# Kernel optimization log

Measured on AMD Instinct MI355X. Metric: run time of the kernel, lower is better.

Reference implementation:

```python
import jax, jax.numpy as jnp
import numpy as np
import math

C = 256
N_HEAD = 8
GROUPS = 16
EPS = 1e-5


def group_norm(x, w, b):
    # x: [B, C, H, W]; biased variance over (group_channels, H, W), like torch GroupNorm
    B, Cc, H, W = x.shape
    xg = x.reshape(B, GROUPS, Cc // GROUPS, H, W)
    mean = xg.mean(axis=(2, 3, 4), keepdims=True)
    var = ((xg - mean) ** 2).mean(axis=(2, 3, 4), keepdims=True)
    xn = ((xg - mean) * jax.lax.rsqrt(var + EPS)).reshape(B, Cc, H, W)
    return xn * w[None, :, None, None] + b[None, :, None, None]


def setup_inputs() -> dict:
    key = jax.random.key(0)
    k0, k1, k2, k3, k4, k5 = jax.random.split(key, 6)
    B, H, W = 4, 48, 48
    input_feat = jax.random.normal(k0, (B, C, H, W), dtype=jnp.float32)
    gn_weight = jnp.ones((C,), dtype=jnp.float32) + 0.02 * jax.random.normal(k1, (C,), dtype=jnp.float32)
    gn_bias = 0.02 * jax.random.normal(k2, (C,), dtype=jnp.float32)
    w_qkv = jax.random.normal(k3, (3 * C, C), dtype=jnp.float32) / math.sqrt(C)  # Conv2d 1x1, no bias
    w_out = jax.random.normal(k4, (C, C), dtype=jnp.float32) / math.sqrt(C)      # Conv2d 1x1
    b_out = 0.02 * jax.random.normal(k5, (C,), dtype=jnp.float32)
    return {"input_feat": input_feat, "gn_weight": gn_weight, "gn_bias": gn_bias,
            "w_qkv": w_qkv, "w_out": w_out, "b_out": b_out}


def reference(input_feat, gn_weight, gn_bias, w_qkv, w_out, b_out):
    # H=W=48 <= max_attn_size=48 -> full attention branch
    B, Cc, H, W = input_feat.shape
    n, d = N_HEAD, Cc // N_HEAD
    S = H * W
    normed = group_norm(input_feat, gn_weight, gn_bias)
    # 1x1 conv QKV: [B, 3C, H, W]
    qkv = jnp.einsum('oc,bchw->bohw', w_qkv, normed)
    # view(B, n, 3*d, H, W).chunk(3, dim=2) == reshape to (B, n, 3, d, S)
    qkv = qkv.reshape(B, n, 3, d, S)
    q, k, v = qkv[:, :, 0], qkv[:, :, 1], qkv[:, :, 2]  # each [B, n, d, S]
    # NOTE: original divides by sqrt(channel), not sqrt(head_dim)
    scale = 1.0 / math.sqrt(Cc)
    scores = jnp.einsum('bnds,bndt->bnst', q, k) * scale  # [B, n, S, S]
    attn = jax.nn.softmax(scores, axis=-1)
    o = jnp.einsum('bnst,bndt->bnds', attn, v)  # [B, n, d, S]
    o = o.reshape(B, Cc, H, W)
    out = jnp.einsum('oc,bchw->bohw', w_out, o) + b_out[None, :, None, None]
    return out + input_feat
```

## Files before the change

kernel.cpp:

```cpp
#include <hip/hip_runtime.h>
#include <hip/hip_bf16.h>
#include <stdint.h>

#define S    2304
#define CHN  256
#define BATCH 4
#define NKEYS 1152
#define QS   0.09016844005556021f

typedef __attribute__((ext_vector_type(8))) short bf16x8;
typedef __attribute__((ext_vector_type(4))) float f32x4;
typedef __attribute__((ext_vector_type(2))) uint32_t u32x2;
typedef __attribute__((ext_vector_type(4))) unsigned short u16x4;
typedef unsigned short u16;

#define AS1 __attribute__((address_space(1)))
#define AS3 __attribute__((address_space(3)))
#define GLDS(gptr, lptr) __builtin_amdgcn_global_load_lds((const AS1 void*)(gptr), (AS3 void*)(lptr), 16, 0, 0)

__device__ __forceinline__ u16 f2bf(float f) {
  union { float f; uint32_t u; } v; v.f = f;
  uint32_t u = v.u;
  u += 0x7fffu + ((u >> 16) & 1u);
  return (u16)(u >> 16);
}
__device__ __forceinline__ float bf2f(u16 h) {
  union { uint32_t u; float f; } v; v.u = ((uint32_t)h) << 16;
  return v.f;
}
__device__ __forceinline__ uint32_t pk_bf16(float a, float b) {
  union { __hip_bfloat162 h; uint32_t u; } cv;
  cv.h = __float22bfloat162_rn(make_float2(a, b));
  return cv.u;
}

__global__ void k_prep(const float* __restrict__ wq, const float* __restrict__ wo,
                       u16* __restrict__ wq_bf, u16* __restrict__ wo_bf,
                       float* __restrict__ sraw) {
  int i = blockIdx.x * 256 + threadIdx.x;
  if (blockIdx.x == 0 && threadIdx.x < 128) sraw[threadIdx.x] = 0.f;
  if (i < 768 * 256) wq_bf[i] = f2bf(wq[i]);
  int j = i - 768 * 256;
  if (j >= 0 && j < 256 * 256) wo_bf[j] = f2bf(wo[j]);
}

__global__ void k_gnstats(const float* __restrict__ x, float* __restrict__ sraw) {
  int blk = blockIdx.x;
  int bg = blk >> 2, part = blk & 3;
  const float4* p = (const float4*)(x + (size_t)bg * 36864) + part * 2304;
  float s = 0.f, ss = 0.f;
  for (int i = threadIdx.x; i < 2304; i += 256) {
    float4 v = p[i];
    s  += v.x + v.y + v.z + v.w;
    ss += v.x * v.x + v.y * v.y + v.z * v.z + v.w * v.w;
  }
  int lane = threadIdx.x & 63, wv = threadIdx.x >> 6;
  for (int m = 1; m < 64; m <<= 1) { s += __shfl_xor(s, m, 64); ss += __shfl_xor(ss, m, 64); }
  __shared__ float rs[4], rss[4];
  if (lane == 0) { rs[wv] = s; rss[wv] = ss; }
  __syncthreads();
  if (threadIdx.x == 0) {
    float S_ = rs[0] + rs[1] + rs[2] + rs[3];
    float SS = rss[0] + rss[1] + rss[2] + rss[3];
    atomicAdd(&sraw[bg * 2], S_);
    atomicAdd(&sraw[bg * 2 + 1], SS);
  }
}

__global__ void k_gnnorm(const float* __restrict__ x, const float* __restrict__ w,
                         const float* __restrict__ bias, const float* __restrict__ sraw,
                         u16* __restrict__ nt) {
  int bid = blockIdx.x;
  int b = bid / 144, r = bid % 144;
  int sblk = r >> 2, cq = r & 3;
  int t = threadIdx.x;
  int ni = t & 63, cgrp = t >> 6;
  int s = sblk * 64 + ni;
  int cbase = cq * 64 + cgrp * 16;
  int bgi = b * 16 + (cbase >> 4);
  float sx = sraw[bgi * 2], ssx = sraw[bgi * 2 + 1];
  float mean = sx * (1.f / 36864.f);
  float var  = ssx * (1.f / 36864.f) - mean * mean;
  float rstd = rsqrtf(var + 1e-5f);
  bf16x8 v0, v1;
  #pragma unroll
  for (int e = 0; e < 16; ++e) {
    int c = cbase + e;
    float val = x[(size_t)(b * 256 + c) * S + s];
    float xn = (val - mean) * rstd * w[c] + bias[c];
    if (e < 8) v0[e] = (short)f2bf(xn); else v1[e - 8] = (short)f2bf(xn);
  }
  u16* dst = nt + (size_t)(b * S + s) * 256 + cbase;
  *(bf16x8*)dst = v0;
  *(bf16x8*)(dst + 8) = v1;
}

__global__ __launch_bounds__(256) void k_qkv(const u16* __restrict__ A,
                                             const u16* __restrict__ Bm,
                                             u16* __restrict__ qkt,
                                             u16* __restrict__ vt) {
  __shared__ __align__(16) u16 As[2][64 * 32];
  __shared__ __align__(16) u16 Bs[2][128 * 32];
  int tid = threadIdx.x, lane = tid & 63, w = tid >> 6;
  int wr = w >> 1, wc = w & 1;
  int cb = lane & 15, q4 = lane >> 4;
  int m0 = blockIdx.y * 64, n0 = blockIdx.x * 128;

  const u16* gA0 = A  + (size_t)(m0 + (tid >> 2)) * 256 + (tid & 3) * 8;
  const u16* gB0 = Bm + (size_t)(n0 + (tid >> 2)) * 256 + (tid & 3) * 8;
  const u16* gB1 = gB0 + 64 * 256;
  char* lA = (char*)&As[0][0] + (w << 10);
  char* lB = (char*)&Bs[0][0] + (w << 10);

  #define STAGE_Q(buf, k0) do {                      \
    GLDS(gA0 + (k0), lA + (buf) * 4096);             \
    GLDS(gB0 + (k0), lB + (buf) * 8192);             \
    GLDS(gB1 + (k0), lB + (buf) * 8192 + 4096);      \
  } while (0)

  f32x4 zero4 = {0.f, 0.f, 0.f, 0.f};
  f32x4 acc[2][4];
  for (int i = 0; i < 2; ++i) for (int j = 0; j < 4; ++j) acc[i][j] = zero4;

  STAGE_Q(0, 0);
  __syncthreads();
  for (int ks = 0; ks < 8; ++ks) {
    int cur = ks & 1;
    if (ks < 7) STAGE_Q(cur ^ 1, (ks + 1) * 32);
    const u16* as = &As[cur][0];
    const u16* bs = &Bs[cur][0];
    bf16x8 af[2], bfr[4];
    for (int i = 0; i < 2; ++i)
      af[i]  = *(const bf16x8*)&as[(wr * 32 + i * 16 + cb) * 32 + 8 * q4];
    for (int j = 0; j < 4; ++j)
      bfr[j] = *(const bf16x8*)&bs[(wc * 64 + j * 16 + cb) * 32 + 8 * q4];
    for (int i = 0; i < 2; ++i)
      for (int j = 0; j < 4; ++j)
        acc[i][j] = __builtin_amdgcn_mfma_f32_16x16x32_bf16(af[i], bfr[j], acc[i][j], 0, 0, 0);
    __syncthreads();
  }

  for (int i = 0; i < 2; ++i)
    for (int j = 0; j < 4; ++j) {
      int ob = m0 + wr * 32 + i * 16 + q4 * 4;
      int n  = n0 + wc * 64 + j * 16 + cb;
      int h = ob / 96, oq = ob % 96;
      if (oq < 64) {
        float sc = (oq < 32) ? QS : 1.f;
        u16x4 pk;
        for (int r = 0; r < 4; ++r) pk[r] = f2bf(acc[i][j][r] * sc);
        *(u16x4*)&qkt[(size_t)n * 512 + h * 64 + oq] = pk;
      } else {
        for (int r = 0; r < 4; ++r)
          vt[(size_t)(h * 32 + oq - 64 + r) * 9216 + n] = f2bf(acc[i][j][r]);
      }
    }
  #undef STAGE_Q
}

__global__ __launch_bounds__(512) void k_attn(const u16* __restrict__ qkt,
                                              const u16* __restrict__ vt,
                                              u16* __restrict__ ot) {
  __shared__ __align__(16) u16 Ks[2][2][2048];
  __shared__ __align__(16) u16 Vd[2][2][2048];
  __shared__ __align__(16) u16 Ps[8][1024];
  __shared__ float Ls[8][16];

  int tid = threadIdx.x, lane = tid & 63, w = tid >> 6;
  int cb = lane & 15, g4 = lane >> 4;
  int qw = w & 3, half = w >> 2;
  int hw = blockIdx.x;
  int orig = (hw & 7) * 144 + (hw >> 3);
  int bh = orig / 36, qtile = orig % 36;
  int b = bh >> 3, h = bh & 7;
  int q0 = qtile * 64 + qw * 16;

  const u16* kbase = qkt + (size_t)(b * S) * 512 + h * 64 + 32 + (size_t)half * NKEYS * 512;
  const u16* vbase = vt + (size_t)(h * 32) * 9216 + (size_t)b * S + half * NKEYS;

  bf16x8 qf = *(const bf16x8*)&qkt[(size_t)(b * S + q0 + cb) * 512 + h * 64 + 8 * g4];
  bf16x8 vones;
  #pragma unroll
  for (int e = 0; e < 8; ++e) vones[e] = (short)0x3F80;

  f32x4 zero4 = {0.f, 0.f, 0.f, 0.f};
  f32x4 acc_o[2]; acc_o[0] = zero4; acc_o[1] = zero4;
  f32x4 lacc4 = zero4;

  int xk = (cb ^ (cb >> 2)) & 3;
  int sw7 = cb & 7;

  const u16* p_kf[4];
  #pragma unroll
  for (int k4 = 0; k4 < 4; ++k4)
    p_kf[k4] = &Ks[half][0][(16 * k4 + cb) * 32 + ((g4 ^ xk) * 8)];
  u16* p_pw[4];
  #pragma unroll
  for (int k4 = 0; k4 < 4; ++k4)
    p_pw[k4] = &Ps[w][cb * 64 + (((2 * k4 + (g4 >> 1)) ^ sw7) << 3) + ((g4 & 1) << 2)];
  const u16* p_pa[2];
  #pragma unroll
  for (int kk = 0; kk < 2; ++kk)
    p_pa[kk] = &Ps[w][cb * 64 + (((4 * kk + g4) ^ sw7) << 3)];
  const u16* p_vb[2][2];
  #pragma unroll
  for (int jd = 0; jd < 2; ++jd)
    #pragma unroll
    for (int kk = 0; kk < 2; ++kk)
      p_vb[jd][kk] = &Vd[half][0][(16 * jd + cb) * 64 + (((4 * kk + g4) ^ sw7) << 3)];

  int tloc = tid & 255;
  int krow = tloc >> 2, kch = (tloc & 3) ^ ((krow ^ (krow >> 2)) & 3);
  int vrow = tloc >> 3, vch = (tloc & 7) ^ (vrow & 7);
  const u16* gK = kbase + (size_t)krow * 512 + kch * 8;
  const u16* gV = vbase + (size_t)vrow * 9216 + vch * 8;
  char* ldsK = (char*)&Ks[half][0][0] + (qw << 10);
  char* ldsV = (char*)&Vd[half][0][0] + (qw << 10);

  #define STAGE_A(buf) do {                          \
    GLDS(gK, ldsK + (buf) * 4096);                   \
    GLDS(gV, ldsV + (buf) * 4096);                   \
    gK += 64 * 512; gV += 64;                        \
  } while (0)

  #define TILE(buf, pf) do {                                                   \
    if (pf) STAGE_A(buf ^ 1);                                                  \
    bf16x8 kf[4];                                                              \
    _Pragma("unroll")                                                          \
    for (int k4 = 0; k4 < 4; ++k4)                                             \
      kf[k4] = *(const bf16x8*)(p_kf[k4] + (buf) * 2048);                      \
    f32x4 pacc[4];                                                             \
    __builtin_amdgcn_s_setprio(1);                                             \
    _Pragma("unroll")                                                          \
    for (int k4 = 0; k4 < 4; ++k4)                                             \
      pacc[k4] = __builtin_amdgcn_mfma_f32_16x16x32_bf16(kf[k4], qf, zero4, 0, 0, 0); \
    __builtin_amdgcn_s_setprio(0);                                             \
    _Pragma("unroll")                                                          \
    for (int k4 = 0; k4 < 4; ++k4) {                                           \
      f32x4 p = pacc[k4];                                                      \
      float e0 = __builtin_amdgcn_exp2f(p[0]);                                 \
      float e1 = __builtin_amdgcn_exp2f(p[1]);                                 \
      float e2 = __builtin_amdgcn_exp2f(p[2]);                                 \
      float e3 = __builtin_amdgcn_exp2f(p[3]);                                 \
      u32x2 pk = { pk_bf16(e0, e1), pk_bf16(e2, e3) };                         \
      *(u32x2*)p_pw[k4] = pk;                                                  \
    }                                                                          \
    asm volatile("s_waitcnt lgkmcnt(0)" ::: "memory");                         \
    __builtin_amdgcn_sched_barrier(0);                                         \
    __builtin_amdgcn_s_setprio(1);                                             \
    bf16x8 pa[2];                                                              \
    _Pragma("unroll")                                                          \
    for (int kk = 0; kk < 2; ++kk)                                             \
      pa[kk] = *(const bf16x8*)p_pa[kk];                                       \
    lacc4 = __builtin_amdgcn_mfma_f32_16x16x32_bf16(pa[0], vones, lacc4, 0, 0, 0); \
    lacc4 = __builtin_amdgcn_mfma_f32_16x16x32_bf16(pa[1], vones, lacc4, 0, 0, 0); \
    _Pragma("unroll")                                                          \
    for (int jd = 0; jd < 2; ++jd)                                             \
      _Pragma("unroll")                                                        \
      for (int kk = 0; kk < 2; ++kk) {                                         \
        bf16x8 vb = *(const bf16x8*)(p_vb[jd][kk] + (buf) * 2048);             \
        acc_o[jd] = __builtin_amdgcn_mfma_f32_16x16x32_bf16(pa[kk], vb, acc_o[jd], 0, 0, 0); \
      }                                                                        \
    __builtin_amdgcn_s_setprio(0);                                             \
    __syncthreads();                                                           \
  } while (0)

  STAGE_A(0);
  __syncthreads();
  for (int it = 0; it < 9; ++it) {
    TILE(0, 1);
    TILE(1, it < 8);
  }

  float* PsF = (float*)&Ps[w][0];
  #pragma unroll
  for (int jd = 0; jd < 2; ++jd)
    *(f32x4*)&PsF[(cb + 16 * jd) * 16 + 4 * g4] = acc_o[jd];
  if (cb == 0)
    *(f32x4*)&Ls[w][4 * g4] = lacc4;
  __syncthreads();

  const float* A0 = (const float*)&Ps[qw][0];
  const float* A1 = (const float*)&Ps[qw + 4][0];
  int dd = half * 16 + cb;
  f32x4 s0 = *(const f32x4*)&A0[dd * 16 + 4 * g4];
  f32x4 s1 = *(const f32x4*)&A1[dd * 16 + 4 * g4];
  f32x4 lt0 = *(const f32x4*)&Ls[qw][4 * g4];
  f32x4 lt1 = *(const f32x4*)&Ls[qw + 4][4 * g4];
  #pragma unroll
  for (int r = 0; r < 4; ++r) {
    float inv = __builtin_amdgcn_rcpf(lt0[r] + lt1[r]);
    int sq = q0 + 4 * g4 + r;
    ot[(size_t)(b * S + sq) * 256 + h * 32 + dd] = f2bf((s0[r] + s1[r]) * inv);
  }
  #undef STAGE_A
  #undef TILE
}

__global__ __launch_bounds__(256) void k_oproj(const u16* __restrict__ A,
                                               const u16* __restrict__ Bm,
                                               float* __restrict__ out,
                                               const float* __restrict__ bias,
                                               const float* __restrict__ resid) {
  __shared__ __align__(16) u16 As[2][64 * 32];
  __shared__ __align__(16) u16 Bs[2][64 * 32];
  int tid = threadIdx.x, lane = tid & 63, w = tid >> 6;
  int cb = lane & 15, q4 = lane >> 4;
  int m0 = blockIdx.y * 64, n0 = blockIdx.x * 64;

  const u16* gA0 = A  + (size_t)(m0 + (tid >> 2)) * 256 + (tid & 3) * 8;
  const u16* gB0 = Bm + (size_t)(n0 + (tid >> 2)) * 256 + (tid & 3) * 8;
  char* lA = (char*)&As[0][0] + (w << 10);
  char* lB = (char*)&Bs[0][0] + (w << 10);

  #define STAGE_O(buf, k0) do {                      \
    GLDS(gA0 + (k0), lA + (buf) * 4096);             \
    GLDS(gB0 + (k0), lB + (buf) * 4096);             \
  } while (0)

  f32x4 zero4 = {0.f, 0.f, 0.f, 0.f};
  f32x4 acc[4];
  for (int j = 0; j < 4; ++j) acc[j] = zero4;

  STAGE_O(0, 0);
  __syncthreads();
  for (int ks = 0; ks < 8; ++ks) {
    int cur = ks & 1;
    if (ks < 7) STAGE_O(cur ^ 1, (ks + 1) * 32);
    const u16* as = &As[cur][0];
    const u16* bs = &Bs[cur][0];
    bf16x8 af = *(const bf16x8*)&as[(w * 16 + cb) * 32 + 8 * q4];
    bf16x8 bfr[4];
    for (int j = 0; j < 4; ++j)
      bfr[j] = *(const bf16x8*)&bs[(j * 16 + cb) * 32 + 8 * q4];
    for (int j = 0; j < 4; ++j)
      acc[j] = __builtin_amdgcn_mfma_f32_16x16x32_bf16(af, bfr[j], acc[j], 0, 0, 0);
    __syncthreads();
  }

  for (int j = 0; j < 4; ++j)
    for (int r = 0; r < 4; ++r) {
      int o = m0 + w * 16 + q4 * 4 + r;
      int n = n0 + j * 16 + cb;
      int b = n / S, s2 = n % S;
      size_t gi = (size_t)(b * 256 + o) * S + s2;
      out[gi] = acc[j][r] + bias[o] + resid[gi];
    }
  #undef STAGE_O
}

extern "C" void kernel_launch(void* const* d_in, const int* in_sizes, int n_in,
                              void* d_out, int out_size, void* d_ws, size_t ws_size,
                              hipStream_t stream) {
  const float* input = (const float*)d_in[0];
  const float* gnw   = (const float*)d_in[1];
  const float* gnb   = (const float*)d_in[2];
  const float* wqkv  = (const float*)d_in[3];
  const float* wout  = (const float*)d_in[4];
  const float* bout  = (const float*)d_in[5];
  float* out = (float*)d_out;
  char* ws = (char*)d_ws;

  size_t o_wq  = 0;
  size_t o_wo  = o_wq + (size_t)768 * 256 * 2;
  size_t o_st  = o_wo + (size_t)256 * 256 * 2;
  size_t o_nt  = o_st + 1024;
  size_t o_qkt = o_nt + (size_t)9216 * 256 * 2;
  size_t o_vt  = o_qkt + (size_t)9216 * 512 * 2;

  u16*    wq_bf = (u16*)(ws + o_wq);
  u16*    wo_bf = (u16*)(ws + o_wo);
  float*  sraw  = (float*)(ws + o_st);
  u16*    nt    = (u16*)(ws + o_nt);
  u16*    qkt   = (u16*)(ws + o_qkt);
  u16*    vt    = (u16*)(ws + o_vt);
  u16*    otb   = (u16*)(ws + o_nt);

  k_prep<<<1024, 256, 0, stream>>>(wqkv, wout, wq_bf, wo_bf, sraw);
  k_gnstats<<<256, 256, 0, stream>>>(input, sraw);
  k_gnnorm<<<576, 256, 0, stream>>>(input, gnw, gnb, sraw, nt);
  k_qkv<<<dim3(72, 12), 256, 0, stream>>>(wq_bf, nt, qkt, vt);
  k_attn<<<1152, 512, 0, stream>>>(qkt, vt, otb);
  k_oproj<<<dim3(144, 4), 256, 0, stream>>>(wo_bf, otb, out, bout, input);
}
```

Measured before the change: 88.82 us.

## Keep softmax probabilities in registers instead of LDS round-trip in attention

The exponentiated scores are no longer written to a per-wave LDS buffer and read back as the A operand of the PV MFMA. The packed bf16 values are rearranged in registers to form the A fragments directly, and the V loads are split into two 4-element halves so the key ordering matches that register layout. This removes LDS stores, the lgkmcnt wait and the sched barrier from each tile and frees the Ps buffer (the epilogue reuses Ks instead). The cost is more, smaller V LDS reads and some register pressure.

```diff
diff --git a/kernel.cpp b/kernel.cpp
--- a/kernel.cpp
+++ b/kernel.cpp
@@ -9,8 +9,9 @@
 #define QS   0.09016844005556021f
 
 typedef __attribute__((ext_vector_type(8))) short bf16x8;
+typedef __attribute__((ext_vector_type(4))) short bf16x4;
 typedef __attribute__((ext_vector_type(4))) float f32x4;
-typedef __attribute__((ext_vector_type(2))) uint32_t u32x2;
+typedef __attribute__((ext_vector_type(4))) uint32_t u32x4;
 typedef __attribute__((ext_vector_type(4))) unsigned short u16x4;
 typedef unsigned short u16;
 
@@ -163,7 +164,6 @@
                                               u16* __restrict__ ot) {
   __shared__ __align__(16) u16 Ks[2][2][2048];
   __shared__ __align__(16) u16 Vd[2][2][2048];
-  __shared__ __align__(16) u16 Ps[8][1024];
   __shared__ float Ls[8][16];
 
   int tid = threadIdx.x, lane = tid & 63, w = tid >> 6;
@@ -188,26 +188,16 @@
   f32x4 lacc4 = zero4;
 
   int xk = (cb ^ (cb >> 2)) & 3;
-  int sw7 = cb & 7;
-
-  const u16* p_kf[4];
-  #pragma unroll
-  for (int k4 = 0; k4 < 4; ++k4)
-    p_kf[k4] = &Ks[half][0][(16 * k4 + cb) * 32 + ((g4 ^ xk) * 8)];
-  u16* p_pw[4];
-  #pragma unroll
-  for (int k4 = 0; k4 < 4; ++k4)
-    p_pw[k4] = &Ps[w][cb * 64 + (((2 * k4 + (g4 >> 1)) ^ sw7) << 3) + ((g4 & 1) << 2)];
-  const u16* p_pa[2];
+
+  const u16* p_k = &Ks[half][0][cb * 32 + ((g4 ^ xk) * 8)];
+  const u16* p_v[2][2];
   #pragma unroll
   for (int kk = 0; kk < 2; ++kk)
-    p_pa[kk] = &Ps[w][cb * 64 + (((4 * kk + g4) ^ sw7) << 3)];
-  const u16* p_vb[2][2];
-  #pragma unroll
-  for (int jd = 0; jd < 2; ++jd)
     #pragma unroll
-    for (int kk = 0; kk < 2; ++kk)
-      p_vb[jd][kk] = &Vd[half][0][(16 * jd + cb) * 64 + (((4 * kk + g4) ^ sw7) << 3)];
+    for (int h2 = 0; h2 < 2; ++h2) {
+      int chunk = 4 * kk + 2 * h2 + (g4 >> 1);
+      p_v[kk][h2] = &Vd[half][0][cb * 64 + ((chunk ^ (cb & 7)) << 3) + 4 * (g4 & 1)];
+    }
 
   int tloc = tid & 255;
   int krow = tloc >> 2, kch = (tloc & 3) ^ ((krow ^ (krow >> 2)) & 3);
@@ -228,13 +218,22 @@
     bf16x8 kf[4];                                                              \
     _Pragma("unroll")                                                          \
     for (int k4 = 0; k4 < 4; ++k4)                                             \
-      kf[k4] = *(const bf16x8*)(p_kf[k4] + (buf) * 2048);                      \
+      kf[k4] = *(const bf16x8*)(p_k + (buf) * 2048 + k4 * 512);                \
+    bf16x4 vlo[2][2], vhi[2][2];                                 \
+    _Pragma("unroll")                                                          \
+    for (int jd = 0; jd < 2; ++jd)                                             \
+      _Pragma("unroll")                                                        \
+      for (int kk = 0; kk < 2; ++kk) {                                         \
+        vlo[jd][kk] = *(const bf16x4*)(p_v[kk][0] + (buf) * 2048 + jd * 1024); \
+        vhi[jd][kk] = *(const bf16x4*)(p_v[kk][1] + (buf) * 2048 + jd * 1024); \
+      }                                                                        \
     f32x4 pacc[4];                                                             \
     __builtin_amdgcn_s_setprio(1);                                             \
     _Pragma("unroll")                                                          \
     for (int k4 = 0; k4 < 4; ++k4)                                             \
       pacc[k4] = __builtin_amdgcn_mfma_f32_16x16x32_bf16(kf[k4], qf, zero4, 0, 0, 0); \
     __builtin_amdgcn_s_setprio(0);                                             \
+    uint32_t W01[4], W23[4];                                                   \
     _Pragma("unroll")                                                          \
     for (int k4 = 0; k4 < 4; ++k4) {                                           \
       f32x4 p = pacc[k4];                                                      \
@@ -242,25 +241,22 @@
       float e1 = __builtin_amdgcn_exp2f(p[1]);                                 \
       float e2 = __builtin_amdgcn_exp2f(p[2]);                                 \
       float e3 = __builtin_amdgcn_exp2f(p[3]);                                 \
-      u32x2 pk = { pk_bf16(e0, e1), pk_bf16(e2, e3) };                         \
-      *(u32x2*)p_pw[k4] = pk;                                                  \
+      W01[k4] = pk_bf16(e0, e1);                                               \
+      W23[k4] = pk_bf16(e2, e3);                                               \
     }                                                                          \
-    asm volatile("s_waitcnt lgkmcnt(0)" ::: "memory");                         \
-    __builtin_amdgcn_sched_barrier(0);                                         \
+    union { u32x4 u; bf16x8 v; } pu0, pu1;                                     \
+    pu0.u = (u32x4){W01[0], W23[0], W01[1], W23[1]};                           \
+    pu1.u = (u32x4){W01[2], W23[2], W01[3], W23[3]};                           \
     __builtin_amdgcn_s_setprio(1);                                             \
-    bf16x8 pa[2];                                                              \
-    _Pragma("unroll")                                                          \
-    for (int kk = 0; kk < 2; ++kk)                                             \
-      pa[kk] = *(const bf16x8*)p_pa[kk];                                       \
-    lacc4 = __builtin_amdgcn_mfma_f32_16x16x32_bf16(pa[0], vones, lacc4, 0, 0, 0); \
-    lacc4 = __builtin_amdgcn_mfma_f32_16x16x32_bf16(pa[1], vones, lacc4, 0, 0, 0); \
-    _Pragma("unroll")                                                          \
-    for (int jd = 0; jd < 2; ++jd)                                             \
-      _Pragma("unroll")                                                        \
-      for (int kk = 0; kk < 2; ++kk) {                                         \
-        bf16x8 vb = *(const bf16x8*)(p_vb[jd][kk] + (buf) * 2048);             \
-        acc_o[jd] = __builtin_amdgcn_mfma_f32_16x16x32_bf16(pa[kk], vb, acc_o[jd], 0, 0, 0); \
-      }                                                                        \
+    lacc4 = __builtin_amdgcn_mfma_f32_16x16x32_bf16(pu0.v, vones, lacc4, 0, 0, 0); \
+    lacc4 = __builtin_amdgcn_mfma_f32_16x16x32_bf16(pu1.v, vones, lacc4, 0, 0, 0); \
+    _Pragma("unroll")                                                          \
+    for (int jd = 0; jd < 2; ++jd) {                                           \
+      bf16x8 vb0 = __builtin_shufflevector(vlo[jd][0], vhi[jd][0], 0,1,2,3,4,5,6,7); \
+      bf16x8 vb1 = __builtin_shufflevector(vlo[jd][1], vhi[jd][1], 0,1,2,3,4,5,6,7); \
+      acc_o[jd] = __builtin_amdgcn_mfma_f32_16x16x32_bf16(pu0.v, vb0, acc_o[jd], 0, 0, 0); \
+      acc_o[jd] = __builtin_amdgcn_mfma_f32_16x16x32_bf16(pu1.v, vb1, acc_o[jd], 0, 0, 0); \
+    }                                                                          \
     __builtin_amdgcn_s_setprio(0);                                             \
     __syncthreads();                                                           \
   } while (0)
@@ -272,16 +268,17 @@
     TILE(1, it < 8);
   }
 
-  float* PsF = (float*)&Ps[w][0];
+  float* OsF = (float*)&Ks[0][0][0];
+  float* myO = OsF + w * 512;
   #pragma unroll
   for (int jd = 0; jd < 2; ++jd)
-    *(f32x4*)&PsF[(cb + 16 * jd) * 16 + 4 * g4] = acc_o[jd];
+    *(f32x4*)&myO[(cb + 16 * jd) * 16 + 4 * g4] = acc_o[jd];
   if (cb == 0)
     *(f32x4*)&Ls[w][4 * g4] = lacc4;
   __syncthreads();
 
-  const float* A0 = (const float*)&Ps[qw][0];
-  const float* A1 = (const float*)&Ps[qw + 4][0];
+  const float* A0 = OsF + qw * 512;
+  const float* A1 = OsF + (qw + 4) * 512;
   int dd = half * 16 + cb;
   f32x4 s0 = *(const f32x4*)&A0[dd * 16 + 4 * g4];
   f32x4 s1 = *(const f32x4*)&A1[dd * 16 + 4 * g4];
```

Result: no change. 88.03 us (-0.9%).
